# Kernel tuning notes

Hardware: AMD Instinct MI355X
Metric: run time of the kernel (lower is better)

## Reference

```python
import jax, jax.numpy as jnp
import numpy as np

DIM = 768
HID = 1536
EPS = 1e-12
SCALE = float(np.sqrt(DIM))


def _layernorm(x, gamma, beta):
    mu = jnp.mean(x, axis=-1, keepdims=True)
    var = jnp.mean(jnp.square(x - mu), axis=-1, keepdims=True)
    return (x - mu) * jax.lax.rsqrt(var + EPS) * gamma + beta


def setup_inputs() -> dict:
    key = jax.random.key(0)
    ks = jax.random.split(key, 16)
    s = 1.0 / np.sqrt(DIM)
    sh = 1.0 / np.sqrt(HID)
    x = jax.random.normal(ks[0], (8, 2048, DIM), dtype=jnp.float32)
    return {
        "x": x,
        "Wq": jax.random.uniform(ks[1], (DIM, DIM), jnp.float32, -s, s),
        "bq": jax.random.uniform(ks[2], (DIM,), jnp.float32, -s, s),
        "Wk": jax.random.uniform(ks[3], (DIM, DIM), jnp.float32, -s, s),
        "bk": jax.random.uniform(ks[4], (DIM,), jnp.float32, -s, s),
        "Wv": jax.random.uniform(ks[5], (DIM, DIM), jnp.float32, -s, s),
        "bv": jax.random.uniform(ks[6], (DIM,), jnp.float32, -s, s),
        "Wp": jax.random.uniform(ks[7], (DIM, DIM), jnp.float32, -s, s),
        "bp": jax.random.uniform(ks[8], (DIM,), jnp.float32, -s, s),
        "g1": jnp.ones((DIM,), jnp.float32),
        "be1": jnp.zeros((DIM,), jnp.float32),
        "W1": jax.random.uniform(ks[9], (HID, DIM), jnp.float32, -s, s),
        "b1": jax.random.uniform(ks[10], (HID,), jnp.float32, -s, s),
        "W2": jax.random.uniform(ks[11], (DIM, HID), jnp.float32, -sh, sh),
        "b2": jax.random.uniform(ks[12], (DIM,), jnp.float32, -sh, sh),
        "g2": jnp.ones((DIM,), jnp.float32),
        "be2": jnp.zeros((DIM,), jnp.float32),
    }


def reference(x, Wq, bq, Wk, bk, Wv, bv, Wp, bp, g1, be1, W1, b1, W2, b2, g2, be2):
    # NOTE: original code does NOT split into heads; single full-dim bmm attention.
    Q = jnp.einsum("bsd,ed->bse", x, Wq) + bq  # [B,S,D]
    K = jnp.einsum("bsd,ed->bse", x, Wk) + bk
    V = jnp.einsum("bsd,ed->bse", x, Wv) + bv
    alpha = jnp.einsum("bqd,bkd->bqk", Q, K) / SCALE  # [B,S,S]
    alpha = jax.nn.softmax(alpha, axis=-1)
    attn = jnp.einsum("bqk,bkd->bqd", alpha, V)
    attn = jnp.einsum("bsd,ed->bse", attn, Wp) + bp  # linear_proj
    h = _layernorm(x + attn, g1, be1)
    mlp = jax.nn.gelu(jnp.einsum("bsd,hd->bsh", h, W1) + b1, approximate=False)
    mlp = jnp.einsum("bsh,dh->bsd", mlp, W2) + b2
    return _layernorm(h + mlp, g2, be2)
```

## Files before the change

### kernel.cpp

```cpp
#include <hip/hip_runtime.h>
#include <math.h>

#define D_MODEL 768
#define D_HID   1536
#define N_BATCH 8
#define SEQLEN  2048
#define NROWS   (N_BATCH*SEQLEN)

typedef unsigned short u16;
typedef unsigned char  u8;
typedef __attribute__((ext_vector_type(8))) short bfrag;
typedef __attribute__((ext_vector_type(4))) float facc;

__device__ __forceinline__ u16 f2bf(float f) {
  unsigned u = __float_as_uint(f);
  u += 0x7fffu + ((u >> 16) & 1u);
  return (u16)(u >> 16);
}
__device__ __forceinline__ float bf2f(u16 u) {
  return __uint_as_float((unsigned)u << 16);
}
__device__ __forceinline__ u8 f2fp8(float f) {
  return (u8)(__builtin_amdgcn_cvt_pk_fp8_f32(f, f, 0, 0) & 0xff);
}

__device__ __forceinline__ void async16(const void* g, void* l) {
  __builtin_amdgcn_global_load_lds((const __attribute__((address_space(1))) void*)g,
                                   (__attribute__((address_space(3))) void*)l,
                                   16, 0, 0);
}
__device__ __forceinline__ void wg_barrier() {
  asm volatile("" ::: "memory");
  __builtin_amdgcn_s_barrier();
  asm volatile("" ::: "memory");
}
#define VMCNT(n) asm volatile("s_waitcnt vmcnt(" #n ")" ::: "memory")

__global__ __launch_bounds__(256) void cvt_all(
    const float* __restrict__ x,  const float* __restrict__ Wq,
    const float* __restrict__ Wk, const float* __restrict__ Wv,
    const float* __restrict__ Wp, const float* __restrict__ W1,
    const float* __restrict__ W2, const float* __restrict__ bq,
    const float* __restrict__ bk, const float* __restrict__ bv,
    u16* __restrict__ XB, u16* __restrict__ WQKV, u16* __restrict__ WPB,
    u16* __restrict__ W1B, u16* __restrict__ W2B, float* __restrict__ BQKV,
    float* __restrict__ LSUM) {
  long i = (long)blockIdx.x * 256 + threadIdx.x;
  const float* src; u16* dst; long off;
  if      (i < 3145728) { src = x;  dst = XB;             off = i; }
  else if (i < 3293184) { src = Wq; dst = WQKV;           off = i - 3145728; }
  else if (i < 3440640) { src = Wk; dst = WQKV + 589824;  off = i - 3293184; }
  else if (i < 3588096) { src = Wv; dst = WQKV + 1179648; off = i - 3440640; }
  else if (i < 3735552) { src = Wp; dst = WPB;            off = i - 3588096; }
  else if (i < 4030464) { src = W1; dst = W1B;            off = i - 3735552; }
  else if (i < 4325376) { src = W2; dst = W2B;            off = i - 4030464; }
  else if (i < 4325952) {
    long j = i - 4325376;
    const float* s = (j < 192) ? bq : (j < 384) ? bk : bv;
    long o = (j < 192) ? j : (j < 384) ? j - 192 : j - 384;
    ((float4*)BQKV)[j] = ((const float4*)s)[o];
    return;
  } else if (i < 4330048) {
    float4 zz = {0.f, 0.f, 0.f, 0.f};
    ((float4*)LSUM)[i - 4325952] = zz;
    return;
  } else return;
  float4 v = ((const float4*)src)[off];
  ushort4 o4;
  o4.x = f2bf(v.x); o4.y = f2bf(v.y); o4.z = f2bf(v.z); o4.w = f2bf(v.w);
  *reinterpret_cast<ushort4*>(dst + off * 4) = o4;
}

enum { EPI_EXP = 1, EPI_DIV = 2, EPI_GELU = 4, EPI_QKV = 5, EPI_RES = 6 };

__global__ __launch_bounds__(512, 2)
void gemm_bt512(const u16* __restrict__ Aall, const u16* __restrict__ Ball,
                void* __restrict__ Cout,
                int M, int N, int K,
                long sA, long sB, long sC,
                const float* __restrict__ bias,
                const u16* __restrict__ residVT,
                float* __restrict__ lsum, float scale)
{
  __shared__ __align__(16) char smem[73728];
  const u16* A = Aall;
  const u16* B = Ball;
  const int bm = blockIdx.x, bn = blockIdx.y;
  const int tid = (int)threadIdx.x;
  const int lane = tid & 63, wv = tid >> 6;
  const int wr = wv >> 2, wc = wv & 3;

  facc acc[4][4] = {};

  const int srow2 = tid >> 2;
  const int c4 = tid & 3;
  const int skey = (srow2 >> 1) & 3;
  const int sc = ((c4 ^ skey) << 3);
  const u16* Abase = A + (long)(bm * 128) * K;
  const u16* Bbase = B + (long)(bn * 256) * K;
  const int fr = lane & 15, g0 = lane >> 4;
  const int rkey = (fr >> 1) & 3;
  const int nt = K >> 5;

  auto STAGE = [&](int t, int b) {
    char* Asb = smem + b * 24576;
    char* Bsb = Asb + 8192;
    const long k0 = (long)t << 5;
    async16(Abase + (long)srow2 * K + k0 + sc, Asb + tid * 16);
#pragma unroll
    for (int p = 0; p < 2; ++p)
      async16(Bbase + (long)(p * 128 + srow2) * K + k0 + sc, Bsb + p * 8192 + tid * 16);
  };

  STAGE(0, 0); STAGE(1, 1);
  int rb_ = 0, sb_ = 2;
  for (int t = 0; t < nt; ++t) {
    if (t < nt - 1) { VMCNT(3); } else { VMCNT(0); }
    wg_barrier();
    if (t + 2 < nt) STAGE(t + 2, sb_);
    const u16* As = (const u16*)(smem + rb_ * 24576);
    const u16* Bs = As + 4096;
    bfrag af[4], bf[4];
#pragma unroll
    for (int i = 0; i < 4; ++i) {
      const int r = wr * 64 + i * 16 + fr;
      af[i] = *(const bfrag*)(As + r * 32 + ((g0 ^ rkey) << 3));
    }
#pragma unroll
    for (int j = 0; j < 4; ++j) {
      const int r = wc * 64 + j * 16 + fr;
      bf[j] = *(const bfrag*)(Bs + r * 32 + ((g0 ^ rkey) << 3));
    }
    __builtin_amdgcn_s_setprio(1);
#pragma unroll
    for (int i = 0; i < 4; ++i)
#pragma unroll
      for (int j = 0; j < 4; ++j)
        acc[i][j] = __builtin_amdgcn_mfma_f32_16x16x32_bf16(af[i], bf[j], acc[i][j], 0, 0, 0);
    __builtin_amdgcn_s_setprio(0);
    rb_ = (rb_ == 2) ? 0 : rb_ + 1;
    sb_ = (sb_ == 2) ? 0 : sb_ + 1;
  }
  wg_barrier();

  const int rb = bm * 128 + wr * 64;
  const int cb = bn * 256 + wc * 64;
  const int quad = lane >> 4;
  const int c64 = bn * 4 + wc;
  const int which = c64 / 12;
  float bj[4];
#pragma unroll
  for (int j = 0; j < 4; ++j) bj[j] = bias[cb + j * 16 + fr];
  if (which == 2) {
    u8* VT_ = (u8*)residVT;
    const int zb = rb >> 11;
    const int seqb = (rb & 2047) + quad * 4;
    const int dimb = (c64 - 24) * 64;
#pragma unroll
    for (int i = 0; i < 4; ++i) {
#pragma unroll
      for (int j = 0; j < 4; ++j) {
        const int dim = dimb + j * 16 + fr;
        unsigned v01 = __builtin_amdgcn_cvt_pk_fp8_f32(acc[i][j][0] + bj[j],
                                                       acc[i][j][1] + bj[j], 0, 0);
        unsigned v23 = __builtin_amdgcn_cvt_pk_fp8_f32(acc[i][j][2] + bj[j],
                                                       acc[i][j][3] + bj[j], 0, 0);
        unsigned w = (v01 & 0xffffu) | (v23 << 16);
        *reinterpret_cast<unsigned*>(VT_ + (long)zb * D_MODEL * SEQLEN +
                                     (long)dim * SEQLEN + seqb + i * 16) = w;
      }
    }
    return;
  }
  u8* ep8 = (u8*)(smem + wv * 8192);
  u8* Cg = (u8*)Cout + (long)which * NROWS * D_MODEL;
  const int cbo = (c64 - which * 12) * 64;
#pragma unroll
  for (int i = 0; i < 4; ++i)
#pragma unroll
    for (int r = 0; r < 4; ++r) {
      const int lrow = i * 16 + quad * 4 + r;
#pragma unroll
      for (int j = 0; j < 4; ++j)
        ep8[lrow * 64 + j * 16 + fr] = f2fp8(acc[i][j][r] + bj[j]);
    }
#pragma unroll
  for (int it = 0; it < 4; ++it) {
    const int lr = it * 16 + (lane >> 2);
    const int ch = (lane & 3) << 4;
    int4 d = *(const int4*)(ep8 + lr * 64 + ch);
    *reinterpret_cast<int4*>(Cg + (long)(rb + lr) * D_MODEL + cbo + ch) = d;
  }
  (void)lsum; (void)scale; (void)M; (void)sA; (void)sB; (void)sC;
}

template<int EPI>
__global__ __launch_bounds__(256, 3)
void gemm_bt(const u16* __restrict__ Aall, const u16* __restrict__ Ball,
             void* __restrict__ Cout,
             int M, int N, int K,
             long sA, long sB, long sC,
             const float* __restrict__ bias,
             const u16* __restrict__ resid,
             float* __restrict__ lsum,
             float scale)
{
  __shared__ __align__(16) char smem[49152];
  const int z = blockIdx.z;
  const u16* A = Aall + (long)z * sA;
  const u16* B = Ball + (long)z * sB;
  const int bm = blockIdx.x, bn = blockIdx.y;
  const int tid = (int)threadIdx.x;
  const int lane = tid & 63, wv = tid >> 6;
  const int wr = wv >> 1, wc = wv & 1;

  facc acc[4][4] = {};

  const int srow2 = tid >> 2;
  const int c4 = tid & 3;
  const int skey = (srow2 >> 1) & 3;
  const int sc = ((c4 ^ skey) << 3);
  const u16* Abase = A + (long)(bm * 128) * K;
  const u16* Bbase = B + (long)(bn * 128) * K;
  const int fr = lane & 15, g0 = lane >> 4;
  const int rkey = (fr >> 1) & 3;
  const int nt = K >> 5;

  auto STAGE = [&](int t, int b) {
    char* Asb = smem + b * 16384;
    char* Bsb = Asb + 8192;
    const long k0 = (long)t << 5;
#pragma unroll
    for (int p = 0; p < 2; ++p) {
      async16(Abase + (long)(p * 64 + srow2) * K + k0 + sc, Asb + p * 4096 + tid * 16);
      async16(Bbase + (long)(p * 64 + srow2) * K + k0 + sc, Bsb + p * 4096 + tid * 16);
    }
  };

  STAGE(0, 0); STAGE(1, 1);
  int rb_ = 0, sb_ = 2;
  for (int t = 0; t < nt; ++t) {
    if (t < nt - 1) { VMCNT(4); } else { VMCNT(0); }
    wg_barrier();
    if (t + 2 < nt) STAGE(t + 2, sb_);
    const u16* As = (const u16*)(smem + rb_ * 16384);
    const u16* Bs = As + 4096;
    bfrag af[4], bf[4];
#pragma unroll
    for (int i = 0; i < 4; ++i) {
      const int r = wr * 64 + i * 16 + fr;
      af[i] = *(const bfrag*)(As + r * 32 + ((g0 ^ rkey) << 3));
    }
#pragma unroll
    for (int j = 0; j < 4; ++j) {
      const int r = wc * 64 + j * 16 + fr;
      bf[j] = *(const bfrag*)(Bs + r * 32 + ((g0 ^ rkey) << 3));
    }
    __builtin_amdgcn_s_setprio(1);
#pragma unroll
    for (int i = 0; i < 4; ++i)
#pragma unroll
      for (int j = 0; j < 4; ++j)
        acc[i][j] = __builtin_amdgcn_mfma_f32_16x16x32_bf16(af[i], bf[j], acc[i][j], 0, 0, 0);
    __builtin_amdgcn_s_setprio(0);
    rb_ = (rb_ == 2) ? 0 : rb_ + 1;
    sb_ = (sb_ == 2) ? 0 : sb_ + 1;
  }
  wg_barrier();

  const int rb = bm * 128 + wr * 64;
  const int cb = bn * 128 + wc * 64;
  const int quad = lane >> 4;

  if constexpr (EPI == EPI_GELU) {
    u16* ep16 = (u16*)(smem + wv * 8192);
    u16* Cg = (u16*)Cout + (long)z * sC;
    float bj[4];
#pragma unroll
    for (int j = 0; j < 4; ++j) bj[j] = bias[cb + j * 16 + fr];
#pragma unroll
    for (int i = 0; i < 4; ++i) {
#pragma unroll
      for (int r = 0; r < 4; ++r) {
        const int lrow = i * 16 + quad * 4 + r;
#pragma unroll
        for (int j = 0; j < 4; ++j) {
          float t = acc[i][j][r] + bj[j];
          float y = 0.7978845608f * (t + 0.044715f * t * t * t);
          float e = __expf(-2.f * fabsf(y));
          float th = (1.f - e) / (1.f + e);
          th = (y < 0.f) ? -th : th;
          ep16[lrow * 64 + j * 16 + fr] = f2bf(0.5f * t * (1.f + th));
        }
      }
    }
#pragma unroll
    for (int it = 0; it < 8; ++it) {
      const int lr = it * 8 + (lane >> 3);
      const int ch = (lane & 7) << 3;
      int4 d = *(const int4*)(ep16 + lr * 64 + ch);
      *reinterpret_cast<int4*>(Cg + (long)(rb + lr) * N + cb + ch) = d;
    }
  } else {
    float* ep32 = (float*)(smem + wv * 8192);
    u16* Cg = (u16*)Cout;
#pragma unroll
    for (int h = 0; h < 2; ++h) {
#pragma unroll
      for (int i2 = 0; i2 < 2; ++i2) {
        const int i = h * 2 + i2;
#pragma unroll
        for (int r = 0; r < 4; ++r) {
          const int lrow = i2 * 16 + quad * 4 + r;
#pragma unroll
          for (int j = 0; j < 4; ++j)
            ep32[lrow * 64 + j * 16 + fr] = acc[i][j][r];
        }
      }
#pragma unroll
      for (int it = 0; it < 8; ++it) {
        const int lr = it * 4 + (lane >> 4);
        const int ch = (lane & 15) << 2;
        float4 d = *(const float4*)(ep32 + lr * 64 + ch);
        const int row = rb + h * 32 + lr;
        const int gcol = cb + ch;
        const long gi = (long)row * N + gcol;
        ushort4 rv = *(const ushort4*)(resid + gi);
        float4 bb = *(const float4*)(bias + gcol);
        ushort4 o;
        o.x = f2bf(d.x + bb.x + bf2f(rv.x));
        o.y = f2bf(d.y + bb.y + bf2f(rv.y));
        o.z = f2bf(d.z + bb.z + bf2f(rv.z));
        o.w = f2bf(d.w + bb.w + bf2f(rv.w));
        *reinterpret_cast<ushort4*>(Cg + gi) = o;
      }
      wg_barrier();
    }
  }
  (void)lsum; (void)scale; (void)M; (void)resid; (void)bias;
}

template<int EPI, int DEPTH>
__global__ __launch_bounds__(256, 6 - DEPTH)
void gemm_f8(const u8* __restrict__ Aall, const u8* __restrict__ Ball,
             void* __restrict__ Cout,
             int M, int N, int K,
             long sA, long sB, long sC,
             float* __restrict__ lsum, float scale)
{
  __shared__ __align__(16) char smem[DEPTH * 16384];
  const int z = blockIdx.z;
  const u8* A = Aall + (long)z * sA;
  const u8* B = Ball + (long)z * sB;
  const int bm = blockIdx.x, bn = blockIdx.y;
  const int tid = (int)threadIdx.x;
  const int lane = tid & 63, wv = tid >> 6;
  const int wr = wv >> 1, wc = wv & 1;

  facc acc[4][4] = {};

  const int srow2 = tid >> 2;
  const int c4 = tid & 3;
  const int skey = (srow2 >> 1) & 3;
  const int scb = ((c4 ^ skey) << 4);
  const u8* Abase = A + (long)(bm * 128) * K;
  const u8* Bbase = B + (long)(bn * 128) * K;
  const int fr = lane & 15, g0 = lane >> 4;
  const int rkey = (fr >> 1) & 3;
  const int nt = K >> 6;

  auto STAGE = [&](int t, int b) {
    char* Asb = smem + b * 16384;
    char* Bsb = Asb + 8192;
    const long k0 = (long)t << 6;
#pragma unroll
    for (int p = 0; p < 2; ++p) {
      async16(Abase + (long)(p * 64 + srow2) * K + k0 + scb, Asb + p * 4096 + tid * 16);
      async16(Bbase + (long)(p * 64 + srow2) * K + k0 + scb, Bsb + p * 4096 + tid * 16);
    }
  };

  auto COMPUTE = [&](int buf) {
    const u8* As = (const u8*)(smem + buf * 16384);
    const u8* Bs = As + 8192;
#pragma unroll
    for (int s = 0; s < 2; ++s) {
      long af[4], bf[4];
      const int cc = (s * 2 + (g0 >> 1)) ^ rkey;
      const int h8 = (g0 & 1) << 3;
#pragma unroll
      for (int i = 0; i < 4; ++i) {
        const int r = wr * 64 + i * 16 + fr;
        af[i] = *(const long*)(As + r * 64 + (cc << 4) + h8);
      }
#pragma unroll
      for (int j = 0; j < 4; ++j) {
        const int r = wc * 64 + j * 16 + fr;
        bf[j] = *(const long*)(Bs + r * 64 + (cc << 4) + h8);
      }
      __builtin_amdgcn_s_setprio(1);
#pragma unroll
      for (int i = 0; i < 4; ++i)
#pragma unroll
        for (int j = 0; j < 4; ++j)
          acc[i][j] = __builtin_amdgcn_mfma_f32_16x16x32_fp8_fp8(af[i], bf[j], acc[i][j], 0, 0, 0);
      __builtin_amdgcn_s_setprio(0);
    }
  };

  if constexpr (DEPTH == 3) {
    STAGE(0, 0); STAGE(1, 1);
    int rb_ = 0, sb_ = 2;
    for (int t = 0; t < nt; ++t) {
      if (t < nt - 1) { VMCNT(4); } else { VMCNT(0); }
      wg_barrier();
      if (t + 2 < nt) STAGE(t + 2, sb_);
      COMPUTE(rb_);
      rb_ = (rb_ == 2) ? 0 : rb_ + 1;
      sb_ = (sb_ == 2) ? 0 : sb_ + 1;
    }
    wg_barrier();
  } else {
    STAGE(0, 0); STAGE(1, 1);
    for (int t = 0; t < nt; ++t) {
      if (t < nt - 1) { VMCNT(4); } else { VMCNT(0); }
      wg_barrier();
      COMPUTE(t & 1);
      wg_barrier();
      if (t + 2 < nt) STAGE(t + 2, t & 1);
    }
  }

  const int rb = bm * 128 + wr * 64;
  const int cb = bn * 128 + wc * 64;
  const int quad = lane >> 4;

  if constexpr (EPI == EPI_EXP) {
    u8* ep8 = (u8*)(smem + wv * 4096);
    u8* Cg = (u8*)Cout + (long)z * sC;
#pragma unroll
    for (int i = 0; i < 4; ++i) {
#pragma unroll
      for (int r = 0; r < 4; ++r) {
        const int lrow = i * 16 + quad * 4 + r;
        const int row = rb + lrow;
        float rs = 0.f;
#pragma unroll
        for (int j = 0; j < 4; ++j) {
          float e = __expf(acc[i][j][r] * scale - 3.0f);
          rs += e;
          ep8[lrow * 64 + j * 16 + fr] = f2fp8(e);
        }
        rs += __shfl_xor(rs, 1);
        rs += __shfl_xor(rs, 2);
        rs += __shfl_xor(rs, 4);
        rs += __shfl_xor(rs, 8);
        if (fr == 0) atomicAdd(&lsum[(long)z * M + row], rs);
      }
    }
#pragma unroll
    for (int it = 0; it < 4; ++it) {
      const int lr = it * 16 + (lane >> 2);
      const int ch = (lane & 3) << 4;
      int4 d = *(const int4*)(ep8 + lr * 64 + ch);
      *reinterpret_cast<int4*>(Cg + (long)(rb + lr) * N + cb + ch) = d;
    }
  } else {
    u16* ep16 = (u16*)(smem + wv * 4096);
    u16* Cg = (u16*)Cout + (long)z * sC;
#pragma unroll
    for (int h = 0; h < 2; ++h) {
#pragma unroll
      for (int i2 = 0; i2 < 2; ++i2) {
        const int i = h * 2 + i2;
#pragma unroll
        for (int r = 0; r < 4; ++r) {
          const int lrow = i2 * 16 + quad * 4 + r;
          const int row = rb + h * 32 + lrow;
          const float inv = 1.f / lsum[(long)z * M + row];
#pragma unroll
          for (int j = 0; j < 4; ++j)
            ep16[lrow * 64 + j * 16 + fr] = f2bf(acc[i][j][r] * inv);
        }
      }
#pragma unroll
      for (int it = 0; it < 4; ++it) {
        const int lr = it * 8 + (lane >> 3);
        const int ch = (lane & 7) << 3;
        int4 d = *(const int4*)(ep16 + lr * 64 + ch);
        *reinterpret_cast<int4*>(Cg + (long)(rb + h * 32 + lr) * N + cb + ch) = d;
      }
      wg_barrier();
    }
  }
}

__global__ __launch_bounds__(192) void layernorm_rows(const u16* __restrict__ in,
                                                      const float* __restrict__ gamma,
                                                      const float* __restrict__ beta,
                                                      float* __restrict__ outf,
                                                      u16* __restrict__ outb) {
  const int row = blockIdx.x;
  const int t = threadIdx.x;
  ushort4 uv = ((const ushort4*)(in + (long)row * D_MODEL))[t];
  float v0 = bf2f(uv.x), v1 = bf2f(uv.y), v2 = bf2f(uv.z), v3 = bf2f(uv.w);
  float s1 = v0 + v1 + v2 + v3;
  float s2 = v0 * v0 + v1 * v1 + v2 * v2 + v3 * v3;
#pragma unroll
  for (int o = 32; o; o >>= 1) { s1 += __shfl_xor(s1, o); s2 += __shfl_xor(s2, o); }
  __shared__ float r1[3], r2[3];
  const int wv = t >> 6, ln = t & 63;
  if (ln == 0) { r1[wv] = s1; r2[wv] = s2; }
  __syncthreads();
  s1 = r1[0] + r1[1] + r1[2];
  s2 = r2[0] + r2[1] + r2[2];
  const float mu = s1 * (1.f / 768.f);
  const float var = s2 * (1.f / 768.f) - mu * mu;
  const float rstd = rsqrtf(var + 1e-12f);
  float4 gv = ((const float4*)gamma)[t];
  float4 bv = ((const float4*)beta)[t];
  float o0 = (v0 - mu) * rstd * gv.x + bv.x;
  float o1 = (v1 - mu) * rstd * gv.y + bv.y;
  float o2 = (v2 - mu) * rstd * gv.z + bv.z;
  float o3 = (v3 - mu) * rstd * gv.w + bv.w;
  if (outf) {
    float4 ov = {o0, o1, o2, o3};
    ((float4*)(outf + (long)row * D_MODEL))[t] = ov;
  }
  if (outb) {
    ushort4 ob;
    ob.x = f2bf(o0); ob.y = f2bf(o1); ob.z = f2bf(o2); ob.w = f2bf(o3);
    ((ushort4*)(outb + (long)row * D_MODEL))[t] = ob;
  }
}

static const size_t OFF_WP   = 0;
static const size_t OFF_W1   = 1179648;
static const size_t OFF_W2   = 3538944;
static const size_t OFF_LSUM = 5898240;
static const size_t OFF_BQKV = 5963776;
static const size_t OFF_QB   = 6291456;
static const size_t OFF_KB   = 18874368;
static const size_t OFF_VT   = 31457280;
static const size_t OFF_EB   = 44040192;
static const size_t OFF_CTX  = 77594624;
static const size_t OFF_XB   = 102760448;
static const size_t OFF_WQKV = 127926272;
static const size_t OFF_M1B  = 131465216;

extern "C" void kernel_launch(void* const* d_in, const int* in_sizes, int n_in,
                              void* d_out, int out_size, void* d_ws, size_t ws_size,
                              hipStream_t stream) {
  const float* x   = (const float*)d_in[0];
  const float* Wq  = (const float*)d_in[1];
  const float* bq  = (const float*)d_in[2];
  const float* Wk  = (const float*)d_in[3];
  const float* bk  = (const float*)d_in[4];
  const float* Wv  = (const float*)d_in[5];
  const float* bv  = (const float*)d_in[6];
  const float* Wp  = (const float*)d_in[7];
  const float* bp  = (const float*)d_in[8];
  const float* g1  = (const float*)d_in[9];
  const float* be1 = (const float*)d_in[10];
  const float* W1  = (const float*)d_in[11];
  const float* b1  = (const float*)d_in[12];
  const float* W2  = (const float*)d_in[13];
  const float* b2  = (const float*)d_in[14];
  const float* g2  = (const float*)d_in[15];
  const float* be2 = (const float*)d_in[16];

  char* ws = (char*)d_ws;
  u16*   WPB  = (u16*)(ws + OFF_WP);
  u16*   W1B  = (u16*)(ws + OFF_W1);
  u16*   W2B  = (u16*)(ws + OFF_W2);
  float* LSUM = (float*)(ws + OFF_LSUM);
  float* BQKV = (float*)(ws + OFF_BQKV);
  u8*    QB   = (u8*)(ws + OFF_QB);
  u8*    KB   = (u8*)(ws + OFF_KB);
  u8*    VT   = (u8*)(ws + OFF_VT);
  u8*    EB   = (u8*)(ws + OFF_EB);
  u16*   CTX  = (u16*)(ws + OFF_CTX);
  u16*   XB   = (u16*)(ws + OFF_XB);
  u16*   WQKV = (u16*)(ws + OFF_WQKV);
  u16*   M1B  = (u16*)(ws + OFF_M1B);
  u16*   PB   = (u16*)(ws + OFF_QB);
  u16*   HB   = (u16*)(ws + OFF_EB);
  u16*   M2B  = (u16*)(ws + OFF_CTX);

  dim3 blk(256), blkg(512), blkl(192);

  cvt_all<<<dim3(16915), blk, 0, stream>>>(x, Wq, Wk, Wv, Wp, W1, W2, bq, bk, bv,
                                           XB, WQKV, WPB, W1B, W2B, BQKV, LSUM);

  gemm_bt512<<<dim3(128, 9, 1), blkg, 0, stream>>>(XB, WQKV, QB,
      NROWS, 3 * D_MODEL, D_MODEL, 0, 0, 0, BQKV, (const u16*)VT, nullptr, 0.f);

  const float sc = 1.0f / sqrtf((float)D_MODEL);
  gemm_f8<EPI_EXP, 2><<<dim3(16, 16, 8), blk, 0, stream>>>(QB, KB, EB,
      SEQLEN, SEQLEN, D_MODEL,
      (long)SEQLEN * D_MODEL, (long)SEQLEN * D_MODEL, (long)SEQLEN * SEQLEN,
      LSUM, sc);
  gemm_f8<EPI_DIV, 3><<<dim3(16, 6, 8), blk, 0, stream>>>(EB, VT, CTX,
      SEQLEN, D_MODEL, SEQLEN,
      (long)SEQLEN * SEQLEN, (long)D_MODEL * SEQLEN, (long)SEQLEN * D_MODEL,
      LSUM, 0.f);
  gemm_bt<EPI_RES><<<dim3(128, 6, 1), blk, 0, stream>>>(CTX, WPB, PB,
      NROWS, D_MODEL, D_MODEL, 0, 0, 0, bp, XB, nullptr, 0.f);
  layernorm_rows<<<dim3(NROWS), blkl, 0, stream>>>(PB, g1, be1, nullptr, HB);
  gemm_bt<EPI_GELU><<<dim3(128, 12, 1), blk, 0, stream>>>(HB, W1B, M1B,
      NROWS, D_HID, D_MODEL, 0, 0, 0, b1, nullptr, nullptr, 0.f);
  gemm_bt<EPI_RES><<<dim3(128, 6, 1), blk, 0, stream>>>(M1B, W2B, M2B,
      NROWS, D_MODEL, D_HID, 0, 0, 0, b2, HB, nullptr, 0.f);
  layernorm_rows<<<dim3(NROWS), blkl, 0, stream>>>(M2B, g2, be2, (float*)d_out, nullptr);

  (void)in_sizes; (void)n_in; (void)out_size; (void)ws_size;
}
```

Measured before the change: 464.4 us.

## Double-buffer LDS fragment reads in GEMM loops with three-stage prefetch

Restructures the main loops of the bf16 512-thread GEMM and the fp8 attention GEMMs. Each loop now issues three global-to-LDS stages up front and is unrolled by two with ping-pong register fragments, so LDS reads for the next k-tile overlap the MFMAs of the current one. The fp8 kernel always uses a 3-deep LDS ring with occupancy hint 3, replacing the per-launch depth template; the QK^T launch moves from depth 2 to 3. This doubles the fragment registers and raises LDS use, which may lower occupancy.

```diff
diff --git a/kernel.cpp b/kernel.cpp
--- a/kernel.cpp
+++ b/kernel.cpp
@@ -35,6 +35,7 @@
   asm volatile("" ::: "memory");
 }
 #define VMCNT(n) asm volatile("s_waitcnt vmcnt(" #n ")" ::: "memory")
+#define LGK0     asm volatile("s_waitcnt lgkmcnt(0)" ::: "memory")
 
 __global__ __launch_bounds__(256) void cvt_all(
     const float* __restrict__ x,  const float* __restrict__ Wq,
@@ -112,36 +113,58 @@
       async16(Bbase + (long)(p * 128 + srow2) * K + k0 + sc, Bsb + p * 8192 + tid * 16);
   };
 
-  STAGE(0, 0); STAGE(1, 1);
-  int rb_ = 0, sb_ = 2;
-  for (int t = 0; t < nt; ++t) {
-    if (t < nt - 1) { VMCNT(3); } else { VMCNT(0); }
+#define RD512(AF, BF, b) do {                                                   \
+    const u16* As_ = (const u16*)(smem + (b) * 24576);                          \
+    const u16* Bs_ = As_ + 4096;                                                \
+    _Pragma("unroll") for (int i = 0; i < 4; ++i) {                             \
+      const int r = wr * 64 + i * 16 + fr;                                      \
+      AF[i] = *(const bfrag*)(As_ + r * 32 + ((g0 ^ rkey) << 3));               \
+    }                                                                           \
+    _Pragma("unroll") for (int j = 0; j < 4; ++j) {                             \
+      const int r = wc * 64 + j * 16 + fr;                                      \
+      BF[j] = *(const bfrag*)(Bs_ + r * 32 + ((g0 ^ rkey) << 3));               \
+    }                                                                           \
+  } while (0)
+
+#define FMA512(AF, BF) do {                                                     \
+    __builtin_amdgcn_s_setprio(1);                                              \
+    _Pragma("unroll") for (int i = 0; i < 4; ++i)                               \
+    _Pragma("unroll") for (int j = 0; j < 4; ++j)                               \
+      acc[i][j] = __builtin_amdgcn_mfma_f32_16x16x32_bf16(AF[i], BF[j],         \
+                                                          acc[i][j], 0, 0, 0); \
+    __builtin_amdgcn_s_setprio(0);                                              \
+  } while (0)
+
+  bfrag afA[4], bfA[4], afB[4], bfB[4];
+  STAGE(0, 0); STAGE(1, 1); STAGE(2, 2);
+  VMCNT(6);
+  wg_barrier();
+  RD512(afA, bfA, 0);
+
+  int bs = 0;
+  int rn = 1;
+  for (int t = 0; t < nt; t += 2) {
+    if (t < nt - 2) { VMCNT(3); } else { VMCNT(0); }
+    LGK0;
     wg_barrier();
-    if (t + 2 < nt) STAGE(t + 2, sb_);
-    const u16* As = (const u16*)(smem + rb_ * 24576);
-    const u16* Bs = As + 4096;
-    bfrag af[4], bf[4];
-#pragma unroll
-    for (int i = 0; i < 4; ++i) {
-      const int r = wr * 64 + i * 16 + fr;
-      af[i] = *(const bfrag*)(As + r * 32 + ((g0 ^ rkey) << 3));
-    }
-#pragma unroll
-    for (int j = 0; j < 4; ++j) {
-      const int r = wc * 64 + j * 16 + fr;
-      bf[j] = *(const bfrag*)(Bs + r * 32 + ((g0 ^ rkey) << 3));
-    }
-    __builtin_amdgcn_s_setprio(1);
-#pragma unroll
-    for (int i = 0; i < 4; ++i)
-#pragma unroll
-      for (int j = 0; j < 4; ++j)
-        acc[i][j] = __builtin_amdgcn_mfma_f32_16x16x32_bf16(af[i], bf[j], acc[i][j], 0, 0, 0);
-    __builtin_amdgcn_s_setprio(0);
-    rb_ = (rb_ == 2) ? 0 : rb_ + 1;
-    sb_ = (sb_ == 2) ? 0 : sb_ + 1;
+    if (t + 3 < nt) STAGE(t + 3, bs);
+    if (t + 1 < nt) RD512(afB, bfB, rn);
+    FMA512(afA, bfA);
+    bs = (bs == 2) ? 0 : bs + 1;
+    rn = (rn == 2) ? 0 : rn + 1;
+    const int u = t + 1;
+    if (u < nt - 2) { VMCNT(3); } else { VMCNT(0); }
+    LGK0;
+    wg_barrier();
+    if (u + 3 < nt) STAGE(u + 3, bs);
+    if (u + 1 < nt) RD512(afA, bfA, rn);
+    FMA512(afB, bfB);
+    bs = (bs == 2) ? 0 : bs + 1;
+    rn = (rn == 2) ? 0 : rn + 1;
   }
   wg_barrier();
+#undef RD512
+#undef FMA512
 
   const int rb = bm * 128 + wr * 64;
   const int cb = bn * 256 + wc * 64;
@@ -340,15 +363,15 @@
   (void)lsum; (void)scale; (void)M; (void)resid; (void)bias;
 }
 
-template<int EPI, int DEPTH>
-__global__ __launch_bounds__(256, 6 - DEPTH)
+template<int EPI>
+__global__ __launch_bounds__(256, 3)
 void gemm_f8(const u8* __restrict__ Aall, const u8* __restrict__ Ball,
              void* __restrict__ Cout,
              int M, int N, int K,
              long sA, long sB, long sC,
              float* __restrict__ lsum, float scale)
 {
-  __shared__ __align__(16) char smem[DEPTH * 16384];
+  __shared__ __align__(16) char smem[49152];
   const int z = blockIdx.z;
   const u8* A = Aall + (long)z * sA;
   const u8* B = Ball + (long)z * sB;
@@ -380,56 +403,62 @@
     }
   };
 
-  auto COMPUTE = [&](int buf) {
-    const u8* As = (const u8*)(smem + buf * 16384);
-    const u8* Bs = As + 8192;
-#pragma unroll
-    for (int s = 0; s < 2; ++s) {
-      long af[4], bf[4];
-      const int cc = (s * 2 + (g0 >> 1)) ^ rkey;
-      const int h8 = (g0 & 1) << 3;
-#pragma unroll
-      for (int i = 0; i < 4; ++i) {
-        const int r = wr * 64 + i * 16 + fr;
-        af[i] = *(const long*)(As + r * 64 + (cc << 4) + h8);
-      }
-#pragma unroll
-      for (int j = 0; j < 4; ++j) {
-        const int r = wc * 64 + j * 16 + fr;
-        bf[j] = *(const long*)(Bs + r * 64 + (cc << 4) + h8);
-      }
-      __builtin_amdgcn_s_setprio(1);
-#pragma unroll
-      for (int i = 0; i < 4; ++i)
-#pragma unroll
-        for (int j = 0; j < 4; ++j)
-          acc[i][j] = __builtin_amdgcn_mfma_f32_16x16x32_fp8_fp8(af[i], bf[j], acc[i][j], 0, 0, 0);
-      __builtin_amdgcn_s_setprio(0);
-    }
-  };
-
-  if constexpr (DEPTH == 3) {
-    STAGE(0, 0); STAGE(1, 1);
-    int rb_ = 0, sb_ = 2;
-    for (int t = 0; t < nt; ++t) {
-      if (t < nt - 1) { VMCNT(4); } else { VMCNT(0); }
-      wg_barrier();
-      if (t + 2 < nt) STAGE(t + 2, sb_);
-      COMPUTE(rb_);
-      rb_ = (rb_ == 2) ? 0 : rb_ + 1;
-      sb_ = (sb_ == 2) ? 0 : sb_ + 1;
-    }
+#define RDF8(AF, BF, b) do {                                                    \
+    const u8* As_ = (const u8*)(smem + (b) * 16384);                            \
+    const u8* Bs_ = As_ + 8192;                                                 \
+    _Pragma("unroll") for (int s = 0; s < 2; ++s) {                             \
+      const int cc = (s * 2 + (g0 >> 1)) ^ rkey;                                \
+      const int h8 = (g0 & 1) << 3;                                             \
+      _Pragma("unroll") for (int i = 0; i < 4; ++i) {                           \
+        const int r = wr * 64 + i * 16 + fr;                                    \
+        AF[s][i] = *(const long*)(As_ + r * 64 + (cc << 4) + h8);               \
+      }                                                                         \
+      _Pragma("unroll") for (int j = 0; j < 4; ++j) {                           \
+        const int r = wc * 64 + j * 16 + fr;                                    \
+        BF[s][j] = *(const long*)(Bs_ + r * 64 + (cc << 4) + h8);               \
+      }                                                                         \
+    }                                                                           \
+  } while (0)
+
+#define FMAF8(AF, BF) do {                                                      \
+    __builtin_amdgcn_s_setprio(1);                                              \
+    _Pragma("unroll") for (int s = 0; s < 2; ++s)                               \
+    _Pragma("unroll") for (int i = 0; i < 4; ++i)                               \
+    _Pragma("unroll") for (int j = 0; j < 4; ++j)                               \
+      acc[i][j] = __builtin_amdgcn_mfma_f32_16x16x32_fp8_fp8(AF[s][i], BF[s][j],\
+                                                             acc[i][j], 0, 0, 0);\
+    __builtin_amdgcn_s_setprio(0);                                              \
+  } while (0)
+
+  long afA[2][4], bfA[2][4], afB[2][4], bfB[2][4];
+  STAGE(0, 0); STAGE(1, 1); STAGE(2, 2);
+  VMCNT(8);
+  wg_barrier();
+  RDF8(afA, bfA, 0);
+
+  int bs = 0, rn = 1;
+  for (int t = 0; t < nt; t += 2) {
+    if (t < nt - 2) { VMCNT(4); } else { VMCNT(0); }
+    LGK0;
     wg_barrier();
-  } else {
-    STAGE(0, 0); STAGE(1, 1);
-    for (int t = 0; t < nt; ++t) {
-      if (t < nt - 1) { VMCNT(4); } else { VMCNT(0); }
-      wg_barrier();
-      COMPUTE(t & 1);
-      wg_barrier();
-      if (t + 2 < nt) STAGE(t + 2, t & 1);
-    }
-  }
+    if (t + 3 < nt) STAGE(t + 3, bs);
+    if (t + 1 < nt) RDF8(afB, bfB, rn);
+    FMAF8(afA, bfA);
+    bs = (bs == 2) ? 0 : bs + 1;
+    rn = (rn == 2) ? 0 : rn + 1;
+    const int u = t + 1;
+    if (u < nt - 2) { VMCNT(4); } else { VMCNT(0); }
+    LGK0;
+    wg_barrier();
+    if (u + 3 < nt) STAGE(u + 3, bs);
+    if (u + 1 < nt) RDF8(afA, bfA, rn);
+    FMAF8(afB, bfB);
+    bs = (bs == 2) ? 0 : bs + 1;
+    rn = (rn == 2) ? 0 : rn + 1;
+  }
+  wg_barrier();
+#undef RDF8
+#undef FMAF8
 
   const int rb = bm * 128 + wr * 64;
   const int cb = bn * 128 + wc * 64;
@@ -596,11 +625,11 @@
       NROWS, 3 * D_MODEL, D_MODEL, 0, 0, 0, BQKV, (const u16*)VT, nullptr, 0.f);
 
   const float sc = 1.0f / sqrtf((float)D_MODEL);
-  gemm_f8<EPI_EXP, 2><<<dim3(16, 16, 8), blk, 0, stream>>>(QB, KB, EB,
+  gemm_f8<EPI_EXP><<<dim3(16, 16, 8), blk, 0, stream>>>(QB, KB, EB,
       SEQLEN, SEQLEN, D_MODEL,
       (long)SEQLEN * D_MODEL, (long)SEQLEN * D_MODEL, (long)SEQLEN * SEQLEN,
       LSUM, sc);
-  gemm_f8<EPI_DIV, 3><<<dim3(16, 6, 8), blk, 0, stream>>>(EB, VT, CTX,
+  gemm_f8<EPI_DIV><<<dim3(16, 6, 8), blk, 0, stream>>>(EB, VT, CTX,
       SEQLEN, D_MODEL, SEQLEN,
       (long)SEQLEN * SEQLEN, (long)D_MODEL * SEQLEN, (long)SEQLEN * D_MODEL,
       LSUM, 0.f);
```

New measurement: 528.0 us. +13.7%, slower.
